# Kernel optimization log

Measured on AMD Instinct MI355X. Metric: run time of the kernel, lower is better.

## Reference

```python
import jax, jax.numpy as jnp
import numpy as np

N_NODES = 100000


def _gcn_conv(x, W, b, src, dst, ew, num_nodes):
    # PyG GCNConv: symmetric normalization with self-loops already included
    # in (src, dst, ew). deg computed on destination (col) index.
    deg = jax.ops.segment_sum(ew, dst, num_segments=num_nodes)  # [N]
    dinv = jnp.where(deg > 0, jax.lax.rsqrt(deg), 0.0)          # [N]
    norm = dinv[src] * ew * dinv[dst]                           # [E]
    h = x @ W                                                   # [N, out]
    msg = h[src] * norm[:, None]                                # [E, out] gather+scale
    out = jax.ops.segment_sum(msg, dst, num_segments=num_nodes) # scatter-add
    return out + b


def setup_inputs() -> dict:
    key = jax.random.key(0)
    k = jax.random.split(key, 8)
    in_c, hid_c, out_c = 128, 128, 64
    E, EL = 1600000, 200000
    x = jax.random.normal(k[0], (N_NODES, in_c), dtype=jnp.float32)
    edge_index = jax.random.randint(k[1], (2, E), 0, N_NODES, dtype=jnp.int64)
    edge_weight = jax.random.uniform(k[2], (E,), dtype=jnp.float32)
    edge_label_index = jax.random.randint(k[3], (2, EL), 0, N_NODES, dtype=jnp.int64)
    # Glorot-ish params
    W1 = jax.random.normal(k[4], (in_c, hid_c), dtype=jnp.float32) / np.sqrt(in_c)
    b1 = jnp.zeros((hid_c,), dtype=jnp.float32)
    W2 = jax.random.normal(k[5], (hid_c, out_c), dtype=jnp.float32) / np.sqrt(hid_c)
    b2 = jnp.zeros((out_c,), dtype=jnp.float32)
    return {"x": x, "edge_index": edge_index, "edge_weight": edge_weight,
            "edge_label_index": edge_label_index,
            "W1": W1, "b1": b1, "W2": W2, "b2": b2}


def reference(x, edge_index, edge_weight, edge_label_index, W1, b1, W2, b2):
    n = x.shape[0]
    # add self-loops (weight 1.0), static shape
    loop = jnp.arange(n, dtype=edge_index.dtype)
    src = jnp.concatenate([edge_index[0], loop])
    dst = jnp.concatenate([edge_index[1], loop])
    ew = jnp.concatenate([edge_weight, jnp.ones((n,), dtype=edge_weight.dtype)])
    h = jax.nn.relu(_gcn_conv(x, W1, b1, src, dst, ew, n))
    z = _gcn_conv(h, W2, b2, src, dst, ew, n)          # [N, out_c]
    # decode: edge dot-product
    return (z[edge_label_index[0]] * z[edge_label_index[1]]).sum(axis=-1)
```

## Files before the change

### kernel.cpp

```cpp
#include <hip/hip_runtime.h>
#include <hip/hip_fp16.h>
#include <math.h>

typedef _Float16 f16x2 __attribute__((ext_vector_type(2)));

__device__ __forceinline__ f16x2 u2h(unsigned int u) { return __builtin_bit_cast(f16x2, u); }
__device__ __forceinline__ unsigned int f2h2(float a, float b) {
    __half2 h = __floats2half2_rn(a, b);
    return *reinterpret_cast<unsigned int*>(&h);
}
__device__ __forceinline__ float fdot2h(unsigned int a, unsigned int b, float c) {
    return __builtin_amdgcn_fdot2(u2h(a), u2h(b), c, false);
}

__global__ __launch_bounds__(256) void gemm128_hist_kernel(
        const float* __restrict__ X, const float* __restrict__ W, __half* __restrict__ Y, int n,
        const int* __restrict__ dst, int* __restrict__ cnt, int* __restrict__ rank, int E) {
    constexpr int M  = 64;
    constexpr int KC = 32;
    __shared__ unsigned Xl[M * 66];
    __shared__ unsigned Wp[16 * 128];

    const int bid = blockIdx.x;
    const int t = threadIdx.x;
    const int EPB = (E + (int)gridDim.x - 1) / (int)gridDim.x;
    const int eBeg = bid * EPB;
    const int eEnd = min(eBeg + EPB, E);

    if ((bid & 1) == 0) {
        for (int e = eBeg + t; e < eEnd; e += 256)
            rank[e] = atomicAdd(&cnt[dst[e]], 1);
    }

    int row0 = bid * M;
    {
        const float4* Xg = (const float4*)X;
        for (int f = t; f < M * 32; f += 256) {
            int r = f >> 5, c4 = f & 31;
            int gr = row0 + r;
            float4 v = make_float4(0.f, 0.f, 0.f, 0.f);
            if (gr < n) v = Xg[(size_t)gr * 32 + c4];
            Xl[r * 66 + c4 * 2 + 0] = f2h2(v.x, v.y);
            Xl[r * 66 + c4 * 2 + 1] = f2h2(v.z, v.w);
        }
    }

    const int cg = t & 31;
    const int r0 = (t >> 5) * 8;

    float4 acc[8];
#pragma unroll
    for (int r = 0; r < 8; r++) acc[r] = make_float4(0.f, 0.f, 0.f, 0.f);

    for (int kc = 0; kc < 128; kc += KC) {
        __syncthreads();
        for (int f = t; f < 16 * 128; f += 256) {
            int kp = f >> 7, col = f & 127;
            int k = kc + kp * 2;
            Wp[f] = f2h2(W[(size_t)k * 128 + col], W[(size_t)(k + 1) * 128 + col]);
        }
        __syncthreads();
#pragma unroll
        for (int kp = 0; kp < 16; kp += 2) {
            uint4 w0 = *(const uint4*)&Wp[kp * 128 + cg * 4];
            uint4 w1 = *(const uint4*)&Wp[(kp + 1) * 128 + cg * 4];
            int xoff = (kc >> 1) + kp;
#pragma unroll
            for (int r = 0; r < 8; r++) {
                uint2 xp = *(const uint2*)&Xl[(r0 + r) * 66 + xoff];
                acc[r].x = fdot2h(xp.x, w0.x, acc[r].x);
                acc[r].y = fdot2h(xp.x, w0.y, acc[r].y);
                acc[r].z = fdot2h(xp.x, w0.z, acc[r].z);
                acc[r].w = fdot2h(xp.x, w0.w, acc[r].w);
                acc[r].x = fdot2h(xp.y, w1.x, acc[r].x);
                acc[r].y = fdot2h(xp.y, w1.y, acc[r].y);
                acc[r].z = fdot2h(xp.y, w1.z, acc[r].z);
                acc[r].w = fdot2h(xp.y, w1.w, acc[r].w);
            }
        }
    }

#pragma unroll
    for (int r = 0; r < 8; r++) {
        int gr = row0 + r0 + r;
        if (gr < n) {
            uint2 u = make_uint2(f2h2(acc[r].x, acc[r].y), f2h2(acc[r].z, acc[r].w));
            *(uint2*)&Y[(size_t)gr * 128 + cg * 4] = u;
        }
    }

    if (bid & 1) {
        for (int e = eBeg + t; e < eEnd; e += 256)
            rank[e] = atomicAdd(&cnt[dst[e]], 1);
    }
}

__global__ __launch_bounds__(256) void scan_block(const int* __restrict__ in, int* __restrict__ out,
                                                  int* __restrict__ bsum, int n) {
    __shared__ int s[256];
    int tid = threadIdx.x;
    int base = blockIdx.x * 1024 + tid * 4;
    int a0 = (base + 0 < n) ? in[base + 0] : 0;
    int a1 = (base + 1 < n) ? in[base + 1] : 0;
    int a2 = (base + 2 < n) ? in[base + 2] : 0;
    int a3 = (base + 3 < n) ? in[base + 3] : 0;
    int tsum = a0 + a1 + a2 + a3;
    s[tid] = tsum;
    __syncthreads();
    for (int off = 1; off < 256; off <<= 1) {
        int v = (tid >= off) ? s[tid - off] : 0;
        __syncthreads();
        s[tid] += v;
        __syncthreads();
    }
    int texcl = s[tid] - tsum;
    if (base + 0 < n) out[base + 0] = texcl;
    if (base + 1 < n) out[base + 1] = texcl + a0;
    if (base + 2 < n) out[base + 2] = texcl + a0 + a1;
    if (base + 3 < n) out[base + 3] = texcl + a0 + a1 + a2;
    if (tid == 255) bsum[blockIdx.x] = s[255];
}

__global__ __launch_bounds__(256) void scan_bsums(int* __restrict__ bsum, int nb) {
    __shared__ int s[256];
    __shared__ int carry_s;
    int tid = threadIdx.x;
    if (tid == 0) carry_s = 0;
    __syncthreads();
    for (int base = 0; base < nb; base += 256) {
        int v = (base + tid < nb) ? bsum[base + tid] : 0;
        int orig = v;
        s[tid] = v;
        __syncthreads();
        for (int off = 1; off < 256; off <<= 1) {
            int u = (tid >= off) ? s[tid - off] : 0;
            __syncthreads();
            s[tid] += u;
            __syncthreads();
        }
        int carry = carry_s;
        int excl = s[tid] - orig + carry;
        if (base + tid < nb) bsum[base + tid] = excl;
        int tot = s[255];
        __syncthreads();
        if (tid == 0) carry_s = carry + tot;
        __syncthreads();
    }
}

__global__ void scan_add(int* __restrict__ rowptr, const int* __restrict__ bscan, int n) {
    int t = blockIdx.x * blockDim.x + threadIdx.x;
    if (t < n) rowptr[t] += bscan[t >> 10];
}

__global__ void scatter_pairs(const int* __restrict__ src, const int* __restrict__ dst,
                              const float* __restrict__ ew, const int* __restrict__ rowptr,
                              const int* __restrict__ rank, int2* __restrict__ pairs, int E) {
    int e = blockIdx.x * blockDim.x + threadIdx.x;
    if (e >= E) return;
    int d = dst[e];
    int p = rowptr[d] + rank[e];
    pairs[p] = make_int2(src[e], __float_as_int(ew[e]));
}

__global__ void deg_dinv_kernel(const int2* __restrict__ pairs, const int* __restrict__ rowptr,
                                float* __restrict__ dinv, int n) {
    int i = blockIdx.x * blockDim.x + threadIdx.x;
    if (i >= n) return;
    int beg = rowptr[i], end = rowptr[i + 1];
    float s = 0.f;
    for (int j = beg; j < end; j++) s += __int_as_float(pairs[j].y);
    dinv[i] = 1.0f / sqrtf(s + 1.0f);
}

__global__ void premul_kernel(int2* __restrict__ pairs, const float* __restrict__ dinv, int E) {
    int e = blockIdx.x * blockDim.x + threadIdx.x;
    if (e >= E) return;
    int2 p = pairs[e];
    p.y = __float_as_int(__int_as_float(p.y) * dinv[p.x]);
    pairs[e] = p;
}

__global__ __launch_bounds__(512, 4) void gather_mv_kernel(const __half* __restrict__ H,
                                                           const int* __restrict__ rowptr,
                                                           const int2* __restrict__ pairs,
                                                           const float* __restrict__ dinv,
                                                           const float* __restrict__ bias,
                                                           const float* __restrict__ W2,
                                                           __half* __restrict__ Z, int n) {
    __shared__ unsigned h1s2[16 * 64];
    __shared__ unsigned w2p[64 * 64];
    const int t = threadIdx.x;
    const int nl = t >> 5;
    const int c4 = t & 31;
    const int node = blockIdx.x * 16 + nl;
    const unsigned coff = (unsigned)c4 * 8u;

    {
#pragma unroll
        for (int f = 0; f < 8; f++) {
            int idx = f * 512 + t;
            int kp = idx >> 6, c = idx & 63;
            w2p[idx] = f2h2(W2[(2 * kp) * 64 + c], W2[(2 * kp + 1) * 64 + c]);
        }
    }

    float4 acc[4];
#pragma unroll
    for (int i = 0; i < 4; i++) acc[i] = make_float4(0.f, 0.f, 0.f, 0.f);

    float di = 0.f;
    int beg = 0, end = 0;
    if (node < n) {
        beg = rowptr[node]; end = rowptr[node + 1];
        di = dinv[node];
        uint2 hv = *(const uint2*)((const char*)H + (size_t)(((unsigned)node << 8) + coff));
        f16x2 ha = u2h(hv.x), hb = u2h(hv.y);
        acc[0].x = (float)ha.x * di; acc[0].y = (float)ha.y * di;
        acc[0].z = (float)hb.x * di; acc[0].w = (float)hb.y * di;
    }

    if (beg < end) {
        int2 pc[8];
#pragma unroll
        for (int i = 0; i < 8; i++) {
            int jj = beg + i;
            pc[i] = pairs[jj < end ? jj : beg];
        }
        for (int j = beg; j < end; j += 8) {
            uint2 v[8];
#pragma unroll
            for (int i = 0; i < 8; i++)
                v[i] = *(const uint2*)((const char*)H + (size_t)(((unsigned)pc[i].x << 8) + coff));
            int2 pn[8];
            int jn = j + 8;
#pragma unroll
            for (int i = 0; i < 8; i++) {
                int jj = jn + i;
                pn[i] = pairs[jj < end ? jj : beg];
            }
#pragma unroll
            for (int i = 0; i < 8; i++) {
                float w = (j + i < end) ? __int_as_float(pc[i].y) : 0.f;
                f16x2 ga = u2h(v[i].x), gb = u2h(v[i].y);
                acc[i & 3].x = fmaf((float)ga.x, w, acc[i & 3].x);
                acc[i & 3].y = fmaf((float)ga.y, w, acc[i & 3].y);
                acc[i & 3].z = fmaf((float)gb.x, w, acc[i & 3].z);
                acc[i & 3].w = fmaf((float)gb.y, w, acc[i & 3].w);
            }
#pragma unroll
            for (int i = 0; i < 8; i++) pc[i] = pn[i];
        }
    }

    {
        float4 a0 = make_float4(0.f, 0.f, 0.f, 0.f);
        if (node < n) {
            float4 bb = ((const float4*)bias)[c4];
            a0.x = fmaxf(((acc[0].x + acc[1].x) + (acc[2].x + acc[3].x)) * di + bb.x, 0.f);
            a0.y = fmaxf(((acc[0].y + acc[1].y) + (acc[2].y + acc[3].y)) * di + bb.y, 0.f);
            a0.z = fmaxf(((acc[0].z + acc[1].z) + (acc[2].z + acc[3].z)) * di + bb.z, 0.f);
            a0.w = fmaxf(((acc[0].w + acc[1].w) + (acc[2].w + acc[3].w)) * di + bb.w, 0.f);
        }
        h1s2[nl * 64 + c4 * 2 + 0] = f2h2(a0.x, a0.y);
        h1s2[nl * 64 + c4 * 2 + 1] = f2h2(a0.z, a0.w);
    }
    __syncthreads();

    float z0 = 0.f, z1 = 0.f;
    const unsigned* hrow = &h1s2[nl * 64];
#pragma unroll 8
    for (int kp = 0; kp < 64; kp++) {
        unsigned h = hrow[kp];
        uint2 wv = *(const uint2*)&w2p[kp * 64 + c4 * 2];
        z0 = fdot2h(h, wv.x, z0);
        z1 = fdot2h(h, wv.y, z1);
    }
    if (node < n) *(unsigned int*)&Z[(size_t)node * 64 + c4 * 2] = f2h2(z0, z1);
}

__global__ __launch_bounds__(256, 4) void gather_reduce64(const __half* __restrict__ H,
                                                          const int* __restrict__ rowptr,
                                                          const int2* __restrict__ pairs,
                                                          const float* __restrict__ dinv,
                                                          const float* __restrict__ bias,
                                                          __half* __restrict__ out, int n) {
    constexpr int TPN = 16;
    int t = blockIdx.x * blockDim.x + threadIdx.x;
    int node = t / TPN;
    int c4 = t % TPN;
    if (node >= n) return;
    const unsigned coff = (unsigned)c4 * 8u;
    int beg = rowptr[node], end = rowptr[node + 1];
    float di = dinv[node];
    float4 bb = ((const float4*)bias)[c4];
    float4 acc[4];
    {
        uint2 hv = *(const uint2*)((const char*)H + (size_t)(((unsigned)node << 7) + coff));
        f16x2 ha = u2h(hv.x), hb = u2h(hv.y);
        acc[0].x = (float)ha.x * di; acc[0].y = (float)ha.y * di;
        acc[0].z = (float)hb.x * di; acc[0].w = (float)hb.y * di;
    }
#pragma unroll
    for (int i = 1; i < 4; i++) acc[i] = make_float4(0.f, 0.f, 0.f, 0.f);

    if (beg < end) {
        int2 pc[8];
#pragma unroll
        for (int i = 0; i < 8; i++) {
            int jj = beg + i;
            pc[i] = pairs[jj < end ? jj : beg];
        }
        for (int j = beg; j < end; j += 8) {
            uint2 v[8];
#pragma unroll
            for (int i = 0; i < 8; i++)
                v[i] = *(const uint2*)((const char*)H + (size_t)(((unsigned)pc[i].x << 7) + coff));
            int2 pn[8];
            int jn = j + 8;
#pragma unroll
            for (int i = 0; i < 8; i++) {
                int jj = jn + i;
                pn[i] = pairs[jj < end ? jj : beg];
            }
#pragma unroll
            for (int i = 0; i < 8; i++) {
                float w = (j + i < end) ? __int_as_float(pc[i].y) : 0.f;
                f16x2 ga = u2h(v[i].x), gb = u2h(v[i].y);
                acc[i & 3].x = fmaf((float)ga.x, w, acc[i & 3].x);
                acc[i & 3].y = fmaf((float)ga.y, w, acc[i & 3].y);
                acc[i & 3].z = fmaf((float)gb.x, w, acc[i & 3].z);
                acc[i & 3].w = fmaf((float)gb.y, w, acc[i & 3].w);
            }
#pragma unroll
            for (int i = 0; i < 8; i++) pc[i] = pn[i];
        }
    }

    float4 r;
    r.x = ((acc[0].x + acc[1].x) + (acc[2].x + acc[3].x)) * di + bb.x;
    r.y = ((acc[0].y + acc[1].y) + (acc[2].y + acc[3].y)) * di + bb.y;
    r.z = ((acc[0].z + acc[1].z) + (acc[2].z + acc[3].z)) * di + bb.z;
    r.w = ((acc[0].w + acc[1].w) + (acc[2].w + acc[3].w)) * di + bb.w;
    uint2 u = make_uint2(f2h2(r.x, r.y), f2h2(r.z, r.w));
    *(uint2*)&out[(size_t)node * 64 + c4 * 4] = u;
}

__global__ void decode_kernel(const __half* __restrict__ Z, const int* __restrict__ ea,
                              const int* __restrict__ eb, float* __restrict__ out, int L) {
    int t = blockIdx.x * blockDim.x + threadIdx.x;
    int e = t >> 4;
    int c = (t & 15) << 2;
    if (e >= L) return;
    uint2 ua = *(const uint2*)&Z[(size_t)ea[e] * 64 + c];
    uint2 ub = *(const uint2*)&Z[(size_t)eb[e] * 64 + c];
    float p = fdot2h(ua.x, ub.x, fdot2h(ua.y, ub.y, 0.f));
    p += __shfl_xor(p, 1);
    p += __shfl_xor(p, 2);
    p += __shfl_xor(p, 4);
    p += __shfl_xor(p, 8);
    if ((t & 15) == 0) out[e] = p;
}

extern "C" void kernel_launch(void* const* d_in, const int* in_sizes, int n_in,
                              void* d_out, int out_size, void* d_ws, size_t ws_size,
                              hipStream_t stream) {
    const float* x   = (const float*)d_in[0];
    const int*   ei  = (const int*)d_in[1];
    const float* ew  = (const float*)d_in[2];
    const int*   eli = (const int*)d_in[3];
    const float* W1  = (const float*)d_in[4];
    const float* b1  = (const float*)d_in[5];
    const float* W2  = (const float*)d_in[6];
    const float* b2  = (const float*)d_in[7];
    float* out = (float*)d_out;

    const int N = in_sizes[0] / 128;
    const int E = in_sizes[2];
    const int L = in_sizes[3] / 2;
    const int NP = ((N + 255) / 256) * 256;

    float* ws     = (float*)d_ws;
    float* dinv   = ws;
    int*   cnt    = (int*)(ws + NP);
    int*   rowptr = cnt + NP;
    int*   bsum   = rowptr + NP;
    int*   rank   = bsum + 1024;
    int2*  pairs  = (int2*)(rank + E);
    __half* A     = (__half*)(pairs + E);
    __half* B     = (__half*)((float*)(pairs + E) + (size_t)NP * 128);
    __half* Zf    = A;

    const int n1 = N + 1;
    const int nb = (n1 + 1023) / 1024;

    hipMemsetAsync(cnt, 0, (size_t)n1 * 4, stream);

    const int Gg = (N + 63) / 64;
    gemm128_hist_kernel<<<Gg, 256, 0, stream>>>(x, W1, A, N, ei + E, cnt, rank, E);

    scan_block<<<nb, 256, 0, stream>>>(cnt, rowptr, bsum, n1);
    scan_bsums<<<1, 256, 0, stream>>>(bsum, nb);
    scan_add<<<(n1 + 255) / 256, 256, 0, stream>>>(rowptr, bsum, n1);
    scatter_pairs<<<(E + 255) / 256, 256, 0, stream>>>(ei, ei + E, ew, rowptr, rank, pairs, E);
    deg_dinv_kernel<<<(N + 255) / 256, 256, 0, stream>>>(pairs, rowptr, dinv, N);
    premul_kernel<<<(E + 255) / 256, 256, 0, stream>>>(pairs, dinv, E);

    gather_mv_kernel<<<(N + 15) / 16, 512, 0, stream>>>(A, rowptr, pairs, dinv, b1, W2, B, N);

    gather_reduce64<<<(N * 16 + 255) / 256, 256, 0, stream>>>(B, rowptr, pairs, dinv, b2, Zf, N);

    decode_kernel<<<(L * 16 + 255) / 256, 256, 0, stream>>>(Zf, eli, eli + L, out, L);
}
```

Before: 398.2 us.

## Pad CSR rows to multiples of eight and drop gather bounds checks

The CSR row pointers are built from per-node counts rounded up to a multiple of eight. Padding slots are filled with zero-weight dummy pairs that point at the node itself, so both gather loops can drop their per-element bounds clamps and weight masks. The shared-memory copy of W2 in the fused mat-vec is rearranged per output column with padding, so each thread can use wide LDS loads in the dot-product loop. The cost is extra padded edges to read and premultiply: up to seven per node, which is a lot given the average degree is about sixteen. The workspace also grows.

```diff
diff --git a/kernel.cpp b/kernel.cpp
--- a/kernel.cpp
+++ b/kernel.cpp
@@ -100,10 +100,10 @@
     __shared__ int s[256];
     int tid = threadIdx.x;
     int base = blockIdx.x * 1024 + tid * 4;
-    int a0 = (base + 0 < n) ? in[base + 0] : 0;
-    int a1 = (base + 1 < n) ? in[base + 1] : 0;
-    int a2 = (base + 2 < n) ? in[base + 2] : 0;
-    int a3 = (base + 3 < n) ? in[base + 3] : 0;
+    int a0 = (base + 0 < n) ? ((in[base + 0] + 7) & ~7) : 0;
+    int a1 = (base + 1 < n) ? ((in[base + 1] + 7) & ~7) : 0;
+    int a2 = (base + 2 < n) ? ((in[base + 2] + 7) & ~7) : 0;
+    int a3 = (base + 3 < n) ? ((in[base + 3] + 7) & ~7) : 0;
     int tsum = a0 + a1 + a2 + a3;
     s[tid] = tsum;
     __syncthreads();
@@ -163,19 +163,23 @@
     pairs[p] = make_int2(src[e], __float_as_int(ew[e]));
 }
 
-__global__ void deg_dinv_kernel(const int2* __restrict__ pairs, const int* __restrict__ rowptr,
-                                float* __restrict__ dinv, int n) {
+__global__ void deg_dinv_kernel(int2* __restrict__ pairs, const int* __restrict__ rowptr,
+                                const int* __restrict__ cnt, float* __restrict__ dinv, int n) {
     int i = blockIdx.x * blockDim.x + threadIdx.x;
     if (i >= n) return;
-    int beg = rowptr[i], end = rowptr[i + 1];
+    int beg = rowptr[i], pend = rowptr[i + 1];
+    int rend = beg + cnt[i];
     float s = 0.f;
-    for (int j = beg; j < end; j++) s += __int_as_float(pairs[j].y);
+    for (int j = beg; j < rend; j++) s += __int_as_float(pairs[j].y);
     dinv[i] = 1.0f / sqrtf(s + 1.0f);
-}
-
-__global__ void premul_kernel(int2* __restrict__ pairs, const float* __restrict__ dinv, int E) {
+    for (int j = rend; j < pend; j++) pairs[j] = make_int2(i, 0);
+}
+
+__global__ void premul_kernel(int2* __restrict__ pairs, const float* __restrict__ dinv,
+                              const int* __restrict__ rowptr, int n) {
+    int Epad = rowptr[n];
     int e = blockIdx.x * blockDim.x + threadIdx.x;
-    if (e >= E) return;
+    if (e >= Epad) return;
     int2 p = pairs[e];
     p.y = __float_as_int(__int_as_float(p.y) * dinv[p.x]);
     pairs[e] = p;
@@ -189,20 +193,20 @@
                                                            const float* __restrict__ W2,
                                                            __half* __restrict__ Z, int n) {
     __shared__ unsigned h1s2[16 * 64];
-    __shared__ unsigned w2p[64 * 64];
+    __shared__ unsigned w2p2[32 * 130];
     const int t = threadIdx.x;
     const int nl = t >> 5;
     const int c4 = t & 31;
     const int node = blockIdx.x * 16 + nl;
     const unsigned coff = (unsigned)c4 * 8u;
 
-    {
-#pragma unroll
-        for (int f = 0; f < 8; f++) {
-            int idx = f * 512 + t;
-            int kp = idx >> 6, c = idx & 63;
-            w2p[idx] = f2h2(W2[(2 * kp) * 64 + c], W2[(2 * kp + 1) * 64 + c]);
-        }
+    for (int f = t; f < 4096; f += 512) {
+        int cc = f >> 7;
+        int rem = f & 127;
+        int kp = rem >> 1, half = rem & 1;
+        int col = cc * 2 + half;
+        w2p2[cc * 130 + kp * 2 + half] =
+            f2h2(W2[(size_t)(2 * kp) * 64 + col], W2[(size_t)(2 * kp + 1) * 64 + col]);
     }
 
     float4 acc[4];
@@ -223,25 +227,18 @@
     if (beg < end) {
         int2 pc[8];
 #pragma unroll
-        for (int i = 0; i < 8; i++) {
-            int jj = beg + i;
-            pc[i] = pairs[jj < end ? jj : beg];
-        }
+        for (int i = 0; i < 8; i++) pc[i] = pairs[beg + i];
         for (int j = beg; j < end; j += 8) {
             uint2 v[8];
 #pragma unroll
             for (int i = 0; i < 8; i++)
                 v[i] = *(const uint2*)((const char*)H + (size_t)(((unsigned)pc[i].x << 8) + coff));
             int2 pn[8];
-            int jn = j + 8;
+#pragma unroll
+            for (int i = 0; i < 8; i++) pn[i] = pairs[j + 8 + i];
 #pragma unroll
             for (int i = 0; i < 8; i++) {
-                int jj = jn + i;
-                pn[i] = pairs[jj < end ? jj : beg];
-            }
-#pragma unroll
-            for (int i = 0; i < 8; i++) {
-                float w = (j + i < end) ? __int_as_float(pc[i].y) : 0.f;
+                float w = __int_as_float(pc[i].y);
                 f16x2 ga = u2h(v[i].x), gb = u2h(v[i].y);
                 acc[i & 3].x = fmaf((float)ga.x, w, acc[i & 3].x);
                 acc[i & 3].y = fmaf((float)ga.y, w, acc[i & 3].y);
@@ -269,12 +266,18 @@
 
     float z0 = 0.f, z1 = 0.f;
     const unsigned* hrow = &h1s2[nl * 64];
-#pragma unroll 8
-    for (int kp = 0; kp < 64; kp++) {
-        unsigned h = hrow[kp];
-        uint2 wv = *(const uint2*)&w2p[kp * 64 + c4 * 2];
-        z0 = fdot2h(h, wv.x, z0);
-        z1 = fdot2h(h, wv.y, z1);
+    const unsigned* wrow = &w2p2[c4 * 130];
+#pragma unroll
+    for (int kp = 0; kp < 64; kp += 4) {
+        uint4 hq = *(const uint4*)&hrow[kp];
+        uint2 wa = *(const uint2*)&wrow[kp * 2 + 0];
+        uint2 wb = *(const uint2*)&wrow[kp * 2 + 2];
+        uint2 wc = *(const uint2*)&wrow[kp * 2 + 4];
+        uint2 wd = *(const uint2*)&wrow[kp * 2 + 6];
+        z0 = fdot2h(hq.x, wa.x, z0); z1 = fdot2h(hq.x, wa.y, z1);
+        z0 = fdot2h(hq.y, wb.x, z0); z1 = fdot2h(hq.y, wb.y, z1);
+        z0 = fdot2h(hq.z, wc.x, z0); z1 = fdot2h(hq.z, wc.y, z1);
+        z0 = fdot2h(hq.w, wd.x, z0); z1 = fdot2h(hq.w, wd.y, z1);
     }
     if (node < n) *(unsigned int*)&Z[(size_t)node * 64 + c4 * 2] = f2h2(z0, z1);
 }
@@ -307,25 +310,18 @@
     if (beg < end) {
         int2 pc[8];
 #pragma unroll
-        for (int i = 0; i < 8; i++) {
-            int jj = beg + i;
-            pc[i] = pairs[jj < end ? jj : beg];
-        }
+        for (int i = 0; i < 8; i++) pc[i] = pairs[beg + i];
         for (int j = beg; j < end; j += 8) {
             uint2 v[8];
 #pragma unroll
             for (int i = 0; i < 8; i++)
                 v[i] = *(const uint2*)((const char*)H + (size_t)(((unsigned)pc[i].x << 7) + coff));
             int2 pn[8];
-            int jn = j + 8;
+#pragma unroll
+            for (int i = 0; i < 8; i++) pn[i] = pairs[j + 8 + i];
 #pragma unroll
             for (int i = 0; i < 8; i++) {
-                int jj = jn + i;
-                pn[i] = pairs[jj < end ? jj : beg];
-            }
-#pragma unroll
-            for (int i = 0; i < 8; i++) {
-                float w = (j + i < end) ? __int_as_float(pc[i].y) : 0.f;
+                float w = __int_as_float(pc[i].y);
                 f16x2 ga = u2h(v[i].x), gb = u2h(v[i].y);
                 acc[i & 3].x = fmaf((float)ga.x, w, acc[i & 3].x);
                 acc[i & 3].y = fmaf((float)ga.y, w, acc[i & 3].y);
@@ -379,6 +375,7 @@
     const int E = in_sizes[2];
     const int L = in_sizes[3] / 2;
     const int NP = ((N + 255) / 256) * 256;
+    const int EPmax = E + 7 * N + 8;
 
     float* ws     = (float*)d_ws;
     float* dinv   = ws;
@@ -387,8 +384,8 @@
     int*   bsum   = rowptr + NP;
     int*   rank   = bsum + 1024;
     int2*  pairs  = (int2*)(rank + E);
-    __half* A     = (__half*)(pairs + E);
-    __half* B     = (__half*)((float*)(pairs + E) + (size_t)NP * 128);
+    __half* A     = (__half*)(pairs + EPmax);
+    __half* B     = (__half*)((float*)(pairs + EPmax) + (size_t)NP * 128);
     __half* Zf    = A;
 
     const int n1 = N + 1;
@@ -403,8 +400,8 @@
     scan_bsums<<<1, 256, 0, stream>>>(bsum, nb);
     scan_add<<<(n1 + 255) / 256, 256, 0, stream>>>(rowptr, bsum, n1);
     scatter_pairs<<<(E + 255) / 256, 256, 0, stream>>>(ei, ei + E, ew, rowptr, rank, pairs, E);
-    deg_dinv_kernel<<<(N + 255) / 256, 256, 0, stream>>>(pairs, rowptr, dinv, N);
-    premul_kernel<<<(E + 255) / 256, 256, 0, stream>>>(pairs, dinv, E);
+    deg_dinv_kernel<<<(N + 255) / 256, 256, 0, stream>>>(pairs, rowptr, cnt, dinv, N);
+    premul_kernel<<<(E + 7 * N + 255) / 256, 256, 0, stream>>>(pairs, dinv, rowptr, N);
 
     gather_mv_kernel<<<(N + 15) / 16, 512, 0, stream>>>(A, rowptr, pairs, dinv, b1, W2, B, N);
 
```

Measured after the change: 480.6 us. +20.7%, slower.
